# Performance work log

Measured on AMD Instinct MI355X. Metric: run time of the kernel, lower is better.

## Reference

```python
import jax, jax.numpy as jnp
import numpy as np

N_NODES = 50000
N_EDGES = 800000
D_IN = 64
D_ID = 32
D_H = 192
D_MSG = 64
D_UP = 128


def _mlp(x, W1, b1, W2, b2):
    # 2-layer MLP: Linear -> ReLU -> Linear (bn=False)
    return jax.nn.relu(x @ W1 + b1) @ W2 + b2


def setup_inputs() -> dict:
    key = jax.random.key(0)
    ks = jax.random.split(key, 16)
    msg_in = 2 * (D_IN + D_ID)   # 192
    upd_in = D_IN + D_MSG        # 128
    s = lambda d: 1.0 / np.sqrt(d)
    return {
        "x": jax.random.normal(ks[0], (N_NODES, D_IN), dtype=jnp.float32),
        "edge_index": jax.random.randint(ks[1], (2, N_EDGES), 0, N_NODES, dtype=jnp.int64),
        "node_centrality": jax.random.uniform(ks[2], (N_NODES,), dtype=jnp.float32),
        "edge_centrality": jax.random.uniform(ks[3], (N_EDGES,), dtype=jnp.float32),
        "identifiers": jax.random.normal(ks[4], (N_NODES, D_ID), dtype=jnp.float32),
        "degrees": jax.random.uniform(ks[5], (N_NODES, 1), dtype=jnp.float32),
        "msg_W1": jax.random.normal(ks[6], (msg_in, D_H), dtype=jnp.float32) * s(msg_in),
        "msg_b1": jnp.zeros((D_H,), dtype=jnp.float32),
        "msg_W2": jax.random.normal(ks[7], (D_H, D_MSG), dtype=jnp.float32) * s(D_H),
        "msg_b2": jnp.zeros((D_MSG,), dtype=jnp.float32),
        "upd_W1": jax.random.normal(ks[8], (upd_in, D_H), dtype=jnp.float32) * s(upd_in),
        "upd_b1": jnp.zeros((D_H,), dtype=jnp.float32),
        "upd_W2": jax.random.normal(ks[9], (D_H, D_UP), dtype=jnp.float32) * s(D_H),
        "upd_b2": jnp.zeros((D_UP,), dtype=jnp.float32),
    }


def reference(x, edge_index, node_centrality, edge_centrality, identifiers, degrees,
              msg_W1, msg_b1, msg_W2, msg_b2, upd_W1, upd_b1, upd_W2, upd_b2):
    n_nodes = x.shape[0]
    # flow='source_to_target' => select=1: i = edge_index[1] (target), j = edge_index[0]
    idx_j = edge_index[0]
    idx_i = edge_index[1]
    x_i, x_j = x[idx_i], x[idx_j]                       # [E, d_in]
    id_i, id_j = identifiers[idx_i], identifiers[idx_j]  # [E, d_id]
    msg_in = jnp.concatenate([x_i, x_j, id_i, id_j], axis=-1)  # [E, 2*(d_in+d_id)]
    msgs = _mlp(msg_in, msg_W1, msg_b1, msg_W2, msg_b2)        # [E, d_msg]
    msgs = msgs * edge_centrality[:, None]
    # torch.sparse.sum over dim 0 of COO([edge_index[0], edge_index[1]]) == segment_sum by edge_index[1]
    agg = jax.ops.segment_sum(msgs, idx_i, num_segments=n_nodes)  # [N, d_msg]
    upd_in = jnp.concatenate([x * node_centrality[:, None], agg], axis=-1)  # [N, d_in+d_msg]
    return _mlp(upd_in, upd_W1, upd_b1, upd_W2, upd_b2)  # [N, d_up]
```

## Files before the change

### kernel.cpp

```cpp
#include <hip/hip_runtime.h>

#define N_NODES 50000
#define N_EDGES 800000
#define NPAD    50048
#define NCHUNK  49

#define EPWAVE 160
#define SLEN   40
#define NITER  10
#define NBLK_E 1250

#define SCAT_BLK 3125
#define PRE_BLK  782

typedef __attribute__((ext_vector_type(8))) _Float16 f16x8;
typedef __attribute__((ext_vector_type(4))) float f32x4;

__global__ __launch_bounds__(256) void k_pack(const float* __restrict__ x,
                                              const float* __restrict__ ids,
                                              const float* __restrict__ mW1,
                                              const float* __restrict__ mW2,
                                              const float* __restrict__ uW1,
                                              const float* __restrict__ uW2,
                                              const int* __restrict__ ei,
                                              int* __restrict__ deg,
                                              _Float16* __restrict__ Xid,
                                              _Float16* __restrict__ W1pk,
                                              _Float16* __restrict__ W2pk,
                                              _Float16* __restrict__ uW1pk,
                                              _Float16* __restrict__ uW2pk) {
    const int tid = blockIdx.x * 256 + threadIdx.x;
    if (tid < N_EDGES) atomicAdd(&deg[ei[N_EDGES + tid]], 1);

    const int XN = NPAD * 96 / 8;
    if (tid < XN) {
        const int n = tid / 12, c0 = (tid % 12) * 8;
        f16x8 v;
#pragma unroll
        for (int i = 0; i < 8; ++i) {
            const int c = c0 + i;
            float f = 0.f;
            if (n < N_NODES) f = (c < 64) ? x[n * 64 + c] : ids[n * 32 + (c - 64)];
            v[i] = (_Float16)f;
        }
        *(f16x8*)&Xid[n * 96 + c0] = v;
        return;
    }
    int r = tid - XN;
    if (r < 3 * 24 * 64) {
        const int kt = r / (24 * 64), nt = (r / 64) % 24, l = r % 64;
        const int e = l & 15, kg = l >> 4;
        f16x8 v;
#pragma unroll
        for (int i = 0; i < 8; ++i) {
            const int k = kt * 32 + kg * 8 + i;
            const int col = nt * 16 + e;
            float val;
            if (col < 192) { const int row = (k < 64) ? k : k + 64;  val = mW1[row * 192 + col]; }
            else           { const int row = (k < 64) ? k + 64 : k + 96; val = mW1[row * 192 + (col - 192)]; }
            v[i] = (_Float16)val;
        }
        *(f16x8*)&W1pk[r * 8] = v;
        return;
    }
    r -= 3 * 24 * 64;
    if (r < 6 * 4 * 64) {
        const int kt = r / (4 * 64), nt = (r / 64) % 4, l = r % 64;
        const int e = l & 15, kg = l >> 4;
        f16x8 v;
#pragma unroll
        for (int i = 0; i < 8; ++i)
            v[i] = (_Float16)mW2[(kt * 32 + kg * 8 + i) * 64 + nt * 16 + e];
        *(f16x8*)&W2pk[r * 8] = v;
        return;
    }
    r -= 6 * 4 * 64;
    if (r < 4 * 12 * 64) {
        const int kt = r / (12 * 64), nt = (r / 64) % 12, l = r % 64;
        const int e = l & 15, kg = l >> 4;
        f16x8 v;
#pragma unroll
        for (int i = 0; i < 8; ++i)
            v[i] = (_Float16)uW1[(kt * 32 + kg * 8 + i) * 192 + nt * 16 + e];
        *(f16x8*)&uW1pk[r * 8] = v;
        return;
    }
    r -= 4 * 12 * 64;
    if (r < 6 * 8 * 64) {
        const int kt = r / (8 * 64), nt = (r / 64) % 8, l = r % 64;
        const int e = l & 15, kg = l >> 4;
        f16x8 v;
#pragma unroll
        for (int i = 0; i < 8; ++i)
            v[i] = (_Float16)uW2[(kt * 32 + kg * 8 + i) * 128 + nt * 16 + e];
        *(f16x8*)&uW2pk[r * 8] = v;
    }
}

__global__ __launch_bounds__(64) void k_scan1(const int* __restrict__ deg,
                                              int* __restrict__ bsum) {
    const int base = blockIdx.x * 1024, l = threadIdx.x;
    int s = 0;
#pragma unroll
    for (int q = 0; q < 16; ++q) {
        const int i = base + q * 64 + l;
        s += (i < NPAD) ? deg[i] : 0;
    }
#pragma unroll
    for (int off = 32; off; off >>= 1) s += __shfl_xor(s, off);
    if (l == 0) bsum[blockIdx.x] = s;
}

__global__ __launch_bounds__(1024) void k_scan3(const int* __restrict__ deg,
                                                const int* __restrict__ bsum,
                                                int* __restrict__ cursor) {
    __shared__ int wtot[16];
    __shared__ int blockBase;
    const int t = threadIdx.x, w = t >> 6, lane = t & 63;
    const int i = blockIdx.x * 1024 + t;
    const int v0 = (i < NPAD) ? deg[i] : 0;
    int v = v0;
#pragma unroll
    for (int off = 1; off < 64; off <<= 1) {
        const int n = __shfl_up(v, off);
        if (lane >= off) v += n;
    }
    if (lane == 63) wtot[w] = v;
    if (w == 0) {
        int bv = (lane < blockIdx.x && lane < NCHUNK) ? bsum[lane] : 0;
#pragma unroll
        for (int off = 32; off; off >>= 1) bv += __shfl_xor(bv, off);
        if (lane == 0) blockBase = bv;
    }
    __syncthreads();
    int wbase = blockBase;
    for (int q = 0; q < w; ++q) wbase += wtot[q];
    if (i < NPAD) cursor[i] = wbase + v - v0;
}

__global__ __launch_bounds__(256) void k_mid(const int* __restrict__ ei,
                                             const float* __restrict__ ec,
                                             int* __restrict__ cursor,
                                             int2* __restrict__ sJI,
                                             float* __restrict__ sEC,
                                             const _Float16* __restrict__ Xid,
                                             const _Float16* __restrict__ W1pk,
                                             const float* __restrict__ b1,
                                             _Float16* __restrict__ P1,
                                             _Float16* __restrict__ P2) {
    if (blockIdx.x < SCAT_BLK) {
        const int e = blockIdx.x * 256 + threadIdx.x;
        if (e >= N_EDGES) return;
        const int i = ei[N_EDGES + e];
        const int pos = atomicAdd(&cursor[i], 1);
        sJI[pos] = make_int2(ei[e], i);
        sEC[pos] = ec[e];
        return;
    }
    const int bid = blockIdx.x - SCAT_BLK;
    const int t = threadIdx.x, w = t >> 6, l = t & 63;
    const int e = l & 15, kg = l >> 4;
    const int n0 = bid * 64 + w * 16;

    f16x8 A[3];
#pragma unroll
    for (int kt = 0; kt < 3; ++kt)
        A[kt] = *(const f16x8*)&Xid[(n0 + e) * 96 + kt * 32 + kg * 8];

#pragma unroll
    for (int nt = 0; nt < 24; ++nt) {
        const float bv = (nt < 12) ? b1[nt * 16 + e] : 0.f;
        f32x4 acc = {bv, bv, bv, bv};
#pragma unroll
        for (int kt = 0; kt < 3; ++kt) {
            const f16x8 B = *(const f16x8*)&W1pk[((kt * 24 + nt) * 64 + l) * 8];
            acc = __builtin_amdgcn_mfma_f32_16x16x32_f16(A[kt], B, acc, 0, 0, 0);
        }
#pragma unroll
        for (int r = 0; r < 4; ++r) {
            const int node = n0 + kg * 4 + r;
            if (node < N_NODES) {
                if (nt < 12) P1[node * 192 + nt * 16 + e] = (_Float16)acc[r];
                else         P2[node * 192 + (nt - 12) * 16 + e] = (_Float16)acc[r];
            }
        }
    }
}

union U16 { uint4 q; f16x8 f; };

#define EDGE_LOAD(A1, A2, JIV)                                                  \
  {                                                                             \
    const _Float16* r1 = P1 + (size_t)(JIV).y * 192 + kg * 8;                   \
    const _Float16* r2 = P2 + (size_t)(JIV).x * 192 + kg * 8;                   \
    _Pragma("unroll")                                                           \
    for (int tt = 0; tt < 6; ++tt) {                                            \
      A1[tt] = *(const uint4*)(r1 + tt * 32);                                   \
      A2[tt] = *(const uint4*)(r2 + tt * 32);                                   \
    }                                                                           \
  }

#define EDGE_COMPUTE(A1, A2, IIV, ITER)                                         \
  {                                                                             \
    f32x4 acc0 = {0.f,0.f,0.f,0.f}, acc1 = {0.f,0.f,0.f,0.f};                   \
    f32x4 acc2 = {0.f,0.f,0.f,0.f}, acc3 = {0.f,0.f,0.f,0.f};                   \
    _Pragma("unroll")                                                           \
    for (int tt = 0; tt < 6; ++tt) {                                            \
      U16 a1, a2;                                                               \
      a1.q = A1[tt]; a2.q = A2[tt];                                             \
      f16x8 hh = a1.f + a2.f;                                                   \
      hh = __builtin_elementwise_max(hh, (f16x8)(_Float16)0.f);                 \
      acc0 = __builtin_amdgcn_mfma_f32_16x16x32_f16(hh, *(const f16x8*)&w2s[(tt*4+0)*64 + l], acc0, 0, 0, 0); \
      acc1 = __builtin_amdgcn_mfma_f32_16x16x32_f16(hh, *(const f16x8*)&w2s[(tt*4+1)*64 + l], acc1, 0, 0, 0); \
      acc2 = __builtin_amdgcn_mfma_f32_16x16x32_f16(hh, *(const f16x8*)&w2s[(tt*4+2)*64 + l], acc2, 0, 0, 0); \
      acc3 = __builtin_amdgcn_mfma_f32_16x16x32_f16(hh, *(const f16x8*)&w2s[(tt*4+3)*64 + l], acc3, 0, 0, 0); \
    }                                                                           \
    const float4 ecq = *(const float4*)(sEC + oBase + (ITER) * 4);              \
    _Pragma("unroll")                                                           \
    for (int r = 0; r < 4; ++r) {                                               \
      const int tr = __shfl((IIV), kg * 4 + r);                                 \
      if (tr != curT) {                                                         \
        if (curT >= 0) {                                                        \
          float* fb = agg + (size_t)curT * 64 + e;                              \
          atomicAdd(fb,      s0); atomicAdd(fb + 16, s1);                       \
          atomicAdd(fb + 32, s2); atomicAdd(fb + 48, s3);                       \
        }                                                                       \
        s0 = s1 = s2 = s3 = 0.f;                                                \
        curT = tr;                                                              \
      }                                                                         \
      const float ecv = ((const float*)&ecq)[r];                                \
      s0 += (acc0[r] + b2v[0]) * ecv;                                           \
      s1 += (acc1[r] + b2v[1]) * ecv;                                           \
      s2 += (acc2[r] + b2v[2]) * ecv;                                           \
      s3 += (acc3[r] + b2v[3]) * ecv;                                           \
    }                                                                           \
  }

__global__ __launch_bounds__(256) void k_edge(const int2* __restrict__ sJI,
                                              const float* __restrict__ sEC,
                                              const _Float16* __restrict__ P1,
                                              const _Float16* __restrict__ P2,
                                              const _Float16* __restrict__ W2pk,
                                              const float* __restrict__ b2,
                                              float* __restrict__ agg) {
    __shared__ uint4 w2s[6 * 4 * 64];
    const int t = threadIdx.x;
    for (int v = t; v < 1536; v += 256) w2s[v] = ((const uint4*)W2pk)[v];
    __syncthreads();

    const int w = t >> 6, l = t & 63;
    const int e = l & 15, kg = l >> 4;
    float b2v[4];
#pragma unroll
    for (int n = 0; n < 4; ++n) b2v[n] = b2[n * 16 + e];

    const int waveBase = (blockIdx.x * 4 + w) * EPWAVE;
    const int aBase = waveBase + (e >> 2) * SLEN + (e & 3);
    const int oBase = waveBase + kg * SLEN;

    int curT = -1;
    float s0 = 0.f, s1 = 0.f, s2 = 0.f, s3 = 0.f;

    int2 jiA = sJI[aBase];
    uint4 A1a[6], A2a[6], A1b[6], A2b[6];
    EDGE_LOAD(A1a, A2a, jiA);

    for (int it = 0; it < NITER; it += 2) {
        const int2 jiB = sJI[aBase + (it + 1) * 4];
        EDGE_LOAD(A1b, A2b, jiB);
        EDGE_COMPUTE(A1a, A2a, jiA.y, it);
        if (it + 2 < NITER) {
            jiA = sJI[aBase + (it + 2) * 4];
            EDGE_LOAD(A1a, A2a, jiA);
        }
        EDGE_COMPUTE(A1b, A2b, jiB.y, it + 1);
    }
    {
        float* fb = agg + (size_t)curT * 64 + e;
        atomicAdd(fb,      s0); atomicAdd(fb + 16, s1);
        atomicAdd(fb + 32, s2); atomicAdd(fb + 48, s3);
    }
}

__global__ __launch_bounds__(256) void k_upd(const _Float16* __restrict__ Xid,
                                             const float* __restrict__ nc,
                                             const float* __restrict__ agg,
                                             const _Float16* __restrict__ uW1pk,
                                             const float* __restrict__ ub1,
                                             const _Float16* __restrict__ uW2pk,
                                             const float* __restrict__ ub2,
                                             float* __restrict__ out) {
    __shared__ char Hs[4][16 * 384];
    const int t = threadIdx.x, w = t >> 6, l = t & 63;
    const int e = l & 15, kg = l >> 4;
    const int n0 = blockIdx.x * 64 + w * 16;
    const int nodeA = n0 + e;

    const float ncv = nc[nodeA < N_NODES ? nodeA : N_NODES - 1];
    f16x8 A[4];
#pragma unroll
    for (int kt = 0; kt < 2; ++kt) {
        const f16x8 xa = *(const f16x8*)&Xid[nodeA * 96 + kt * 32 + kg * 8];
        f16x8 o;
#pragma unroll
        for (int i = 0; i < 8; ++i) o[i] = (_Float16)((float)xa[i] * ncv);
        A[kt] = o;
    }
#pragma unroll
    for (int kt = 2; kt < 4; ++kt) {
        const float* ap = agg + (size_t)nodeA * 64 + (kt - 2) * 32 + kg * 8;
        const float4 a0 = *(const float4*)ap;
        const float4 a1 = *(const float4*)(ap + 4);
        f16x8 o;
        o[0] = (_Float16)a0.x; o[1] = (_Float16)a0.y; o[2] = (_Float16)a0.z; o[3] = (_Float16)a0.w;
        o[4] = (_Float16)a1.x; o[5] = (_Float16)a1.y; o[6] = (_Float16)a1.z; o[7] = (_Float16)a1.w;
        A[kt] = o;
    }

#pragma unroll
    for (int nt = 0; nt < 12; ++nt) {
        const float bv = ub1[nt * 16 + e];
        f32x4 acc = {bv, bv, bv, bv};
#pragma unroll
        for (int kt = 0; kt < 4; ++kt) {
            const f16x8 B = *(const f16x8*)&uW1pk[((kt * 12 + nt) * 64 + l) * 8];
            acc = __builtin_amdgcn_mfma_f32_16x16x32_f16(A[kt], B, acc, 0, 0, 0);
        }
#pragma unroll
        for (int r = 0; r < 4; ++r) {
            const int hr = kg * 4 + r;
            const float v = acc[r] > 0.f ? acc[r] : 0.f;
            int byte = hr * 384 + (nt * 16 + e) * 2;
            byte ^= (hr & 7) << 4;
            *(_Float16*)(&Hs[w][0] + byte) = (_Float16)v;
        }
    }

    f16x8 A2[6];
#pragma unroll
    for (int kt = 0; kt < 6; ++kt) {
        int byte = e * 384 + kt * 64 + kg * 16;
        byte ^= (e & 7) << 4;
        A2[kt] = *(const f16x8*)(&Hs[w][0] + byte);
    }
#pragma unroll
    for (int nt = 0; nt < 8; ++nt) {
        const float bv = ub2[nt * 16 + e];
        f32x4 acc = {bv, bv, bv, bv};
#pragma unroll
        for (int kt = 0; kt < 6; ++kt) {
            const f16x8 B = *(const f16x8*)&uW2pk[((kt * 8 + nt) * 64 + l) * 8];
            acc = __builtin_amdgcn_mfma_f32_16x16x32_f16(A2[kt], B, acc, 0, 0, 0);
        }
#pragma unroll
        for (int r = 0; r < 4; ++r) {
            const int node = n0 + kg * 4 + r;
            if (node < N_NODES) out[node * 128 + nt * 16 + e] = acc[r];
        }
    }
}

extern "C" void kernel_launch(void* const* d_in, const int* in_sizes, int n_in,
                              void* d_out, int out_size, void* d_ws, size_t ws_size,
                              hipStream_t stream) {
    const float* x   = (const float*)d_in[0];
    const int*   ei  = (const int*)d_in[1];
    const float* ncv = (const float*)d_in[2];
    const float* ecv = (const float*)d_in[3];
    const float* ids = (const float*)d_in[4];
    const float* mW1 = (const float*)d_in[6];
    const float* mb1 = (const float*)d_in[7];
    const float* mW2 = (const float*)d_in[8];
    const float* mb2 = (const float*)d_in[9];
    const float* uW1 = (const float*)d_in[10];
    const float* ub1 = (const float*)d_in[11];
    const float* uW2 = (const float*)d_in[12];
    const float* ub2 = (const float*)d_in[13];
    float* out = (float*)d_out;

    char* ws = (char*)d_ws;
    _Float16*       Xid  = (_Float16*)ws;         ws += (size_t)NPAD * 96 * 2;
    _Float16*       P1   = (_Float16*)ws;         ws += (size_t)NPAD * 192 * 2;
    _Float16*       P2   = (_Float16*)ws;         ws += (size_t)NPAD * 192 * 2;
    float*          agg  = (float*)ws;            ws += (size_t)NPAD * 64 * 4;
    _Float16*       W1pk = (_Float16*)ws;         ws += 3 * 24 * 64 * 8 * 2;
    _Float16*       W2pk = (_Float16*)ws;         ws += 6 * 4 * 64 * 8 * 2;
    _Float16*       uW1pk= (_Float16*)ws;         ws += 4 * 12 * 64 * 8 * 2;
    _Float16*       uW2pk= (_Float16*)ws;         ws += 6 * 8 * 64 * 8 * 2;
    int*            deg  = (int*)ws;              ws += (size_t)NPAD * 4;
    int*            cur  = (int*)ws;              ws += (size_t)NPAD * 4;
    int*            bsum = (int*)ws;              ws += 64 * 4;
    int2*           sJI  = (int2*)ws;             ws += (size_t)N_EDGES * 8;
    float*          sEC  = (float*)ws;            ws += (size_t)N_EDGES * 4;

    hipMemsetAsync(agg, 0, (size_t)NPAD * 64 * sizeof(float), stream);
    hipMemsetAsync(deg, 0, (size_t)NPAD * sizeof(int), stream);

    const int packGrid = (N_EDGES + 255) / 256;
    k_pack<<<packGrid, 256, 0, stream>>>(x, ids, mW1, mW2, uW1, uW2, ei, deg,
                                         Xid, W1pk, W2pk, uW1pk, uW2pk);
    k_scan1<<<NCHUNK, 64, 0, stream>>>(deg, bsum);
    k_scan3<<<NCHUNK, 1024, 0, stream>>>(deg, bsum, cur);
    k_mid<<<SCAT_BLK + PRE_BLK, 256, 0, stream>>>(ei, ecv, cur, sJI, sEC,
                                                  Xid, W1pk, mb1, P1, P2);
    k_edge<<<NBLK_E, 256, 0, stream>>>(sJI, sEC, P1, P2, W2pk, mb2, agg);
    k_upd<<<NPAD / 64, 256, 0, stream>>>(Xid, ncv, agg, uW1pk, ub1, uW2pk, ub2, out);
}
```

Before: 247.6 us.

## Fold fp16 node packing into precompute, merge scan kernels, zero agg in scatter

The fp32 x/identifier to fp16 conversion moves out of k_pack into k_mid's node-precompute path, which now reads fp32 directly and writes a slimmer 64-column fp16 x copy for the update kernel. The two-kernel scan becomes a single kernel where each block re-sums all preceding degrees itself. The agg memset is replaced by zeroing inside the scatter blocks of k_mid. Together these remove one launch, one memset and an intermediate round trip through memory, at the cost of redundant prefix summing in later scan blocks.

```diff
diff --git a/kernel.cpp b/kernel.cpp
--- a/kernel.cpp
+++ b/kernel.cpp
@@ -16,15 +16,12 @@
 typedef __attribute__((ext_vector_type(8))) _Float16 f16x8;
 typedef __attribute__((ext_vector_type(4))) float f32x4;
 
-__global__ __launch_bounds__(256) void k_pack(const float* __restrict__ x,
-                                              const float* __restrict__ ids,
-                                              const float* __restrict__ mW1,
+__global__ __launch_bounds__(256) void k_pack(const float* __restrict__ mW1,
                                               const float* __restrict__ mW2,
                                               const float* __restrict__ uW1,
                                               const float* __restrict__ uW2,
                                               const int* __restrict__ ei,
                                               int* __restrict__ deg,
-                                              _Float16* __restrict__ Xid,
                                               _Float16* __restrict__ W1pk,
                                               _Float16* __restrict__ W2pk,
                                               _Float16* __restrict__ uW1pk,
@@ -32,21 +29,7 @@
     const int tid = blockIdx.x * 256 + threadIdx.x;
     if (tid < N_EDGES) atomicAdd(&deg[ei[N_EDGES + tid]], 1);
 
-    const int XN = NPAD * 96 / 8;
-    if (tid < XN) {
-        const int n = tid / 12, c0 = (tid % 12) * 8;
-        f16x8 v;
-#pragma unroll
-        for (int i = 0; i < 8; ++i) {
-            const int c = c0 + i;
-            float f = 0.f;
-            if (n < N_NODES) f = (c < 64) ? x[n * 64 + c] : ids[n * 32 + (c - 64)];
-            v[i] = (_Float16)f;
-        }
-        *(f16x8*)&Xid[n * 96 + c0] = v;
-        return;
-    }
-    int r = tid - XN;
+    int r = tid;
     if (r < 3 * 24 * 64) {
         const int kt = r / (24 * 64), nt = (r / 64) % 24, l = r % 64;
         const int e = l & 15, kg = l >> 4;
@@ -97,26 +80,19 @@
     }
 }
 
-__global__ __launch_bounds__(64) void k_scan1(const int* __restrict__ deg,
-                                              int* __restrict__ bsum) {
-    const int base = blockIdx.x * 1024, l = threadIdx.x;
-    int s = 0;
-#pragma unroll
-    for (int q = 0; q < 16; ++q) {
-        const int i = base + q * 64 + l;
-        s += (i < NPAD) ? deg[i] : 0;
-    }
-#pragma unroll
-    for (int off = 32; off; off >>= 1) s += __shfl_xor(s, off);
-    if (l == 0) bsum[blockIdx.x] = s;
-}
-
-__global__ __launch_bounds__(1024) void k_scan3(const int* __restrict__ deg,
-                                                const int* __restrict__ bsum,
-                                                int* __restrict__ cursor) {
+__global__ __launch_bounds__(1024) void k_scan(const int* __restrict__ deg,
+                                               int* __restrict__ cursor) {
     __shared__ int wtot[16];
-    __shared__ int blockBase;
+    __shared__ int pre[16];
     const int t = threadIdx.x, w = t >> 6, lane = t & 63;
+
+    int partial = 0;
+    const int lim = blockIdx.x * 1024;
+    for (int i = t; i < lim; i += 1024) partial += deg[i];
+#pragma unroll
+    for (int off = 32; off; off >>= 1) partial += __shfl_xor(partial, off);
+    if (lane == 0) pre[w] = partial;
+
     const int i = blockIdx.x * 1024 + t;
     const int v0 = (i < NPAD) ? deg[i] : 0;
     int v = v0;
@@ -126,16 +102,13 @@
         if (lane >= off) v += n;
     }
     if (lane == 63) wtot[w] = v;
-    if (w == 0) {
-        int bv = (lane < blockIdx.x && lane < NCHUNK) ? bsum[lane] : 0;
-#pragma unroll
-        for (int off = 32; off; off >>= 1) bv += __shfl_xor(bv, off);
-        if (lane == 0) blockBase = bv;
-    }
     __syncthreads();
-    int wbase = blockBase;
-    for (int q = 0; q < w; ++q) wbase += wtot[q];
-    if (i < NPAD) cursor[i] = wbase + v - v0;
+
+    int base = 0;
+#pragma unroll
+    for (int q = 0; q < 16; ++q) base += pre[q];
+    for (int q = 0; q < w; ++q) base += wtot[q];
+    if (i < NPAD) cursor[i] = base + v - v0;
 }
 
 __global__ __launch_bounds__(256) void k_mid(const int* __restrict__ ei,
@@ -143,14 +116,19 @@
                                              int* __restrict__ cursor,
                                              int2* __restrict__ sJI,
                                              float* __restrict__ sEC,
-                                             const _Float16* __restrict__ Xid,
+                                             const float* __restrict__ x,
+                                             const float* __restrict__ ids,
                                              const _Float16* __restrict__ W1pk,
                                              const float* __restrict__ b1,
                                              _Float16* __restrict__ P1,
-                                             _Float16* __restrict__ P2) {
+                                             _Float16* __restrict__ P2,
+                                             _Float16* __restrict__ Xid64,
+                                             float* __restrict__ agg) {
     if (blockIdx.x < SCAT_BLK) {
         const int e = blockIdx.x * 256 + threadIdx.x;
-        if (e >= N_EDGES) return;
+        const float4 z = {0.f, 0.f, 0.f, 0.f};
+        *(float4*)&agg[e * 4] = z;
+        if (e < 768) *(float4*)&agg[3200000 + e * 4] = z;
         const int i = ei[N_EDGES + e];
         const int pos = atomicAdd(&cursor[i], 1);
         sJI[pos] = make_int2(ei[e], i);
@@ -161,11 +139,28 @@
     const int t = threadIdx.x, w = t >> 6, l = t & 63;
     const int e = l & 15, kg = l >> 4;
     const int n0 = bid * 64 + w * 16;
+    const int node = n0 + e;
+    const bool valid = node < N_NODES;
 
     f16x8 A[3];
 #pragma unroll
-    for (int kt = 0; kt < 3; ++kt)
-        A[kt] = *(const f16x8*)&Xid[(n0 + e) * 96 + kt * 32 + kg * 8];
+    for (int kt = 0; kt < 3; ++kt) {
+        float4 f0 = {0.f, 0.f, 0.f, 0.f}, f1 = {0.f, 0.f, 0.f, 0.f};
+        if (valid) {
+            if (kt < 2) {
+                f0 = *(const float4*)&x[node * 64 + kt * 32 + kg * 8];
+                f1 = *(const float4*)&x[node * 64 + kt * 32 + kg * 8 + 4];
+            } else {
+                f0 = *(const float4*)&ids[node * 32 + kg * 8];
+                f1 = *(const float4*)&ids[node * 32 + kg * 8 + 4];
+            }
+        }
+        f16x8 v;
+        v[0] = (_Float16)f0.x; v[1] = (_Float16)f0.y; v[2] = (_Float16)f0.z; v[3] = (_Float16)f0.w;
+        v[4] = (_Float16)f1.x; v[5] = (_Float16)f1.y; v[6] = (_Float16)f1.z; v[7] = (_Float16)f1.w;
+        A[kt] = v;
+        if (kt < 2) *(f16x8*)&Xid64[node * 64 + kt * 32 + kg * 8] = v;
+    }
 
 #pragma unroll
     for (int nt = 0; nt < 24; ++nt) {
@@ -178,10 +173,10 @@
         }
 #pragma unroll
         for (int r = 0; r < 4; ++r) {
-            const int node = n0 + kg * 4 + r;
-            if (node < N_NODES) {
-                if (nt < 12) P1[node * 192 + nt * 16 + e] = (_Float16)acc[r];
-                else         P2[node * 192 + (nt - 12) * 16 + e] = (_Float16)acc[r];
+            const int onode = n0 + kg * 4 + r;
+            if (onode < N_NODES) {
+                if (nt < 12) P1[onode * 192 + nt * 16 + e] = (_Float16)acc[r];
+                else         P2[onode * 192 + (nt - 12) * 16 + e] = (_Float16)acc[r];
             }
         }
     }
@@ -282,7 +277,7 @@
     }
 }
 
-__global__ __launch_bounds__(256) void k_upd(const _Float16* __restrict__ Xid,
+__global__ __launch_bounds__(256) void k_upd(const _Float16* __restrict__ Xid64,
                                              const float* __restrict__ nc,
                                              const float* __restrict__ agg,
                                              const _Float16* __restrict__ uW1pk,
@@ -300,7 +295,7 @@
     f16x8 A[4];
 #pragma unroll
     for (int kt = 0; kt < 2; ++kt) {
-        const f16x8 xa = *(const f16x8*)&Xid[nodeA * 96 + kt * 32 + kg * 8];
+        const f16x8 xa = *(const f16x8*)&Xid64[nodeA * 64 + kt * 32 + kg * 8];
         f16x8 o;
 #pragma unroll
         for (int i = 0; i < 8; ++i) o[i] = (_Float16)((float)xa[i] * ncv);
@@ -379,7 +374,7 @@
     float* out = (float*)d_out;
 
     char* ws = (char*)d_ws;
-    _Float16*       Xid  = (_Float16*)ws;         ws += (size_t)NPAD * 96 * 2;
+    _Float16*       Xid64= (_Float16*)ws;         ws += (size_t)NPAD * 64 * 2;
     _Float16*       P1   = (_Float16*)ws;         ws += (size_t)NPAD * 192 * 2;
     _Float16*       P2   = (_Float16*)ws;         ws += (size_t)NPAD * 192 * 2;
     float*          agg  = (float*)ws;            ws += (size_t)NPAD * 64 * 4;
@@ -389,20 +384,17 @@
     _Float16*       uW2pk= (_Float16*)ws;         ws += 6 * 8 * 64 * 8 * 2;
     int*            deg  = (int*)ws;              ws += (size_t)NPAD * 4;
     int*            cur  = (int*)ws;              ws += (size_t)NPAD * 4;
-    int*            bsum = (int*)ws;              ws += 64 * 4;
     int2*           sJI  = (int2*)ws;             ws += (size_t)N_EDGES * 8;
     float*          sEC  = (float*)ws;            ws += (size_t)N_EDGES * 4;
 
-    hipMemsetAsync(agg, 0, (size_t)NPAD * 64 * sizeof(float), stream);
     hipMemsetAsync(deg, 0, (size_t)NPAD * sizeof(int), stream);
 
-    const int packGrid = (N_EDGES + 255) / 256;
-    k_pack<<<packGrid, 256, 0, stream>>>(x, ids, mW1, mW2, uW1, uW2, ei, deg,
-                                         Xid, W1pk, W2pk, uW1pk, uW2pk);
-    k_scan1<<<NCHUNK, 64, 0, stream>>>(deg, bsum);
-    k_scan3<<<NCHUNK, 1024, 0, stream>>>(deg, bsum, cur);
+    k_pack<<<(N_EDGES + 255) / 256, 256, 0, stream>>>(mW1, mW2, uW1, uW2, ei, deg,
+                                                      W1pk, W2pk, uW1pk, uW2pk);
+    k_scan<<<NCHUNK, 1024, 0, stream>>>(deg, cur);
     k_mid<<<SCAT_BLK + PRE_BLK, 256, 0, stream>>>(ei, ecv, cur, sJI, sEC,
-                                                  Xid, W1pk, mb1, P1, P2);
+                                                  x, ids, W1pk, mb1, P1, P2,
+                                                  Xid64, agg);
     k_edge<<<NBLK_E, 256, 0, stream>>>(sJI, sEC, P1, P2, W2pk, mb2, agg);
-    k_upd<<<NPAD / 64, 256, 0, stream>>>(Xid, ncv, agg, uW1pk, ub1, uW2pk, ub2, out);
-}
+    k_upd<<<PRE_BLK, 256, 0, stream>>>(Xid64, ncv, agg, uW1pk, ub1, uW2pk, ub2, out);
+}
```

After: 234.0 us (median of 2 runs). 5.5% less time.
